# Kernel optimization log

Hardware: AMD Instinct MI355X
Metric: run time of the kernel (lower is better)

The kernel has to match this reference:

```python
import jax, jax.numpy as jnp
import numpy as np

N_WORDS = 8192   # total words across all concepts
L = 24           # chars per word (padded)
D = 256          # word_vec_d
H = 8            # attention heads
DFF = 1024
VOCAB = 128
N_CONCEPTS = 1024
MAXW = 16        # max_words
GROUPS = 4       # n_names: 4 equal groups of concepts


def setup_inputs() -> dict:
    key = jax.random.key(0)
    ks = jax.random.split(key, 9)
    rng = np.random.default_rng(0)
    # char tokens in [1, VOCAB), ragged word lengths in [4, L], tail = 0 (pad)
    vals = rng.integers(1, VOCAB, size=(N_WORDS, L))
    lens = rng.integers(4, L + 1, size=(N_WORDS,))
    inputs = np.where(np.arange(L)[None, :] < lens[:, None], vals, 0)
    # ragged words-per-concept: alternate 4 / 12 -> sums to N_WORDS, <= MAXW
    counts = np.where(np.arange(N_CONCEPTS) % 2 == 0, 4, 12)
    concept_id = np.repeat(np.arange(N_CONCEPTS), counts)
    word_pos = np.concatenate([np.arange(c) for c in counts])

    def w(k, shape):
        return 0.02 * jax.random.normal(k, shape, jnp.float32)

    return {
        "inputs": jnp.asarray(inputs, jnp.int32),
        "concept_id": jnp.asarray(concept_id, jnp.int32),
        "word_pos": jnp.asarray(word_pos, jnp.int32),
        "n_concepts": N_CONCEPTS,
        "n_names": GROUPS,
        "we_emb": w(ks[0], (VOCAB, D)),
        "we_qkv": w(ks[1], (D, 3 * D)),
        "we_o": w(ks[2], (D, D)),
        "we_ff1": w(ks[3], (D, DFF)),
        "we_ff2": w(ks[4], (DFF, D)),
        "ne_qkv": w(ks[5], (D, 3 * D)),
        "ne_o": w(ks[6], (D, D)),
        "ne_ff1": w(ks[7], (D, DFF)),
        "ne_ff2": w(ks[8], (DFF, D)),
    }


def _ln(x):
    m = x.mean(-1, keepdims=True)
    v = ((x - m) ** 2).mean(-1, keepdims=True)
    return (x - m) * jax.lax.rsqrt(v + 1e-5)


def _mha(x, wqkv, wo, key_pad=None):
    n, l, d = x.shape
    hd = d // H
    q, k, v = jnp.split(x @ wqkv, 3, axis=-1)
    q = q.reshape(n, l, H, hd)
    k = k.reshape(n, l, H, hd)
    v = v.reshape(n, l, H, hd)
    s = jnp.einsum('nqhd,nkhd->nhqk', q, k) / jnp.sqrt(jnp.asarray(hd, x.dtype))
    if key_pad is not None:
        s = jnp.where(key_pad[:, None, None, :], -1e9, s)
    a = jax.nn.softmax(s, axis=-1)
    o = jnp.einsum('nhqk,nkhd->nqhd', a, v).reshape(n, l, d)
    return o @ wo


def _block(x, wqkv, wo, w1, w2, key_pad=None):
    h = _ln(x + _mha(x, wqkv, wo, key_pad))
    return _ln(h + jax.nn.relu(h @ w1) @ w2)


def reference(inputs, concept_id, word_pos, n_concepts, n_names,
              we_emb, we_qkv, we_o, we_ff1, we_ff2,
              ne_qkv, ne_o, ne_ff1, ne_ff2):
    pad_mask = inputs == 0  # [N_WORDS, L]
    x = we_emb[inputs]      # [N_WORDS, L, D]
    word_ft = _block(x, we_qkv, we_o, we_ff1, we_ff2, pad_mask)
    # masked mean over chars -> one vector per word
    np_mask = (~pad_mask)[..., None].astype(word_ft.dtype)  # [N_WORDS, L, 1]
    name_vec = (word_ft * np_mask).sum(1) / np_mask.sum(1)   # [N_WORDS, D]
    # ragged -> padded: one scatter instead of per-sample torch.cat
    padded = jnp.zeros((n_concepts, MAXW, name_vec.shape[-1]), name_vec.dtype)
    padded = padded.at[concept_id, word_pos].set(name_vec)   # [n_concepts, MAXW, D]
    name_ft = _block(padded, ne_qkv, ne_o, ne_ff1, ne_ff2)
    row_pad = (padded == 0).all(-1, keepdims=True)           # all-zero rows = pad words
    name_ft = jnp.where(row_pad, jnp.zeros((), name_ft.dtype), name_ft)
    counts = (name_ft != 0).sum(1).astype(name_ft.dtype)     # [n_concepts, D]
    pooled = name_ft.sum(1) / counts                         # [n_concepts, D]
    return tuple(jnp.split(pooled, n_names, axis=0))
```

## Files before the change

### kernel.cpp

```cpp
#include <hip/hip_runtime.h>
#include <hip/hip_bf16.h>

#define NWORDS 8192
#define LW 24
#define DIM 256
#define NHEAD 8
#define DFF 1024
#define NCONC 1024
#define MAXW 16
#define TN (NCONC * MAXW)

typedef float floatx4 __attribute__((ext_vector_type(4)));
typedef short shortx8 __attribute__((ext_vector_type(8)));

__device__ __forceinline__ float bf2f(ushort u) {
  union { uint u; float f; } v; v.u = ((uint)u) << 16; return v.f;
}
__device__ __forceinline__ ushort f2bf(float f) {
  union { float f; uint u; } v; v.f = f;
  return (ushort)((v.u + 0x7FFFu + ((v.u >> 16) & 1u)) >> 16);
}

__device__ __forceinline__ void load_lds16(const ushort* gsrc, ushort* lds) {
  __builtin_amdgcn_global_load_lds((const __attribute__((address_space(1))) void*)gsrc,
                                   (__attribute__((address_space(3))) void*)lds, 16, 0, 0);
}

#define WAIT_VM0() __builtin_amdgcn_s_waitcnt(0x0F70)
#define WAIT_LGKM0() __builtin_amdgcn_s_waitcnt(0xC07F)

#define STAGE_COL(lane) ((((lane) & 3) ^ (((lane) >> 3) & 3)) * 8)
#define FRAG_OFF(row, quad) (((row) * 32) + ((((quad) ^ (((row) >> 1) & 3))) * 8))

__global__ __launch_bounds__(256) void wprep(const float* __restrict__ W,
                                             ushort* __restrict__ WT, int K, int N) {
  int idx = blockIdx.x * 256 + threadIdx.x;
  if (idx < K * N) {
    int k = idx / N, n = idx % N;
    WT[n * K + k] = f2bf(W[idx]);
  }
}

__global__ __launch_bounds__(256) void embed4(const int* __restrict__ inputs,
                                              const float* __restrict__ we_emb,
                                              ushort* __restrict__ x, int ntok) {
  int idx = blockIdx.x * 256 + threadIdx.x;
  int t = idx >> 6, d = (idx & 63) * 4;
  if (t < ntok) {
    const float4 f = *(const float4*)&we_emb[inputs[t] * DIM + d];
    uint2 o;
    o.x = (uint)f2bf(f.x) | ((uint)f2bf(f.y) << 16);
    o.y = (uint)f2bf(f.z) | ((uint)f2bf(f.w) << 16);
    *(uint2*)&x[(size_t)t * DIM + d] = o;
  }
}

template <bool RELU>
__global__ __launch_bounds__(256) void gemm128(const ushort* __restrict__ A,
                                               const ushort* __restrict__ BT,
                                               ushort* __restrict__ C,
                                               int lda, int ldb, int ldc, int K) {
  __shared__ ushort As[2][128 * 32];
  __shared__ ushort Bs[2][128 * 32];
  const int tid = threadIdx.x;
  const int w = tid >> 6, lane = tid & 63;
  const int quad = lane >> 4, l16 = lane & 15;
  const long m0 = (long)blockIdx.y * 128;
  const long n0 = (long)blockIdx.x * 128;
  const int srow = lane >> 2;
  const int scol = STAGE_COL(lane);
  const int wr = (w >> 1) * 64, wc = (w & 1) * 64;

  floatx4 acc[4][4] = {};
  for (int k0 = 0; k0 < K; k0 += 64) {
#pragma unroll
    for (int s = 0; s < 2; s++)
#pragma unroll
      for (int i = 0; i < 2; i++) {
        int r = w * 32 + i * 16;
        load_lds16(&A[(m0 + r + srow) * lda + k0 + s * 32 + scol], &As[s][r * 32]);
        load_lds16(&BT[(n0 + r + srow) * ldb + k0 + s * 32 + scol], &Bs[s][r * 32]);
      }
    __syncthreads();
#pragma unroll
    for (int s = 0; s < 2; s++) {
      shortx8 a[4], b[4];
#pragma unroll
      for (int i = 0; i < 4; i++) a[i] = *(const shortx8*)&As[s][FRAG_OFF(wr + i * 16 + l16, quad)];
#pragma unroll
      for (int j = 0; j < 4; j++) b[j] = *(const shortx8*)&Bs[s][FRAG_OFF(wc + j * 16 + l16, quad)];
#pragma unroll
      for (int i = 0; i < 4; i++)
#pragma unroll
        for (int j = 0; j < 4; j++)
          acc[i][j] = __builtin_amdgcn_mfma_f32_16x16x32_bf16(a[i], b[j], acc[i][j], 0, 0, 0);
    }
    __syncthreads();
  }
#pragma unroll
  for (int i = 0; i < 4; i++)
#pragma unroll
    for (int j = 0; j < 4; j++)
#pragma unroll
      for (int r = 0; r < 4; r++) {
        float v = acc[i][j][r];
        if (RELU) v = fmaxf(v, 0.f);
        long m = m0 + wr + i * 16 + quad * 4 + r;
        long n = n0 + wc + j * 16 + l16;
        C[m * ldc + n] = f2bf(v);
      }
}

__global__ __launch_bounds__(256) void gemm_ln64(const ushort* __restrict__ A, int lda,
                                                 const ushort* __restrict__ BT,
                                                 const ushort* __restrict__ RES,
                                                 ushort* __restrict__ C,
                                                 int K) {
  __shared__ ushort As[2][64 * 32];
  __shared__ ushort Bs[2][256 * 32];
  __shared__ float red1[64 * 4];
  __shared__ float red2[64 * 4];
  const int tid = threadIdx.x;
  const int w = tid >> 6, lane = tid & 63;
  const int quad = lane >> 4, l16 = lane & 15;
  const long m0 = (long)blockIdx.x * 64;
  const int srow = lane >> 2;
  const int scol = STAGE_COL(lane);
  const int wc = w * 64;

  floatx4 acc[4][4] = {};
  for (int k0 = 0; k0 < K; k0 += 64) {
#pragma unroll
    for (int s = 0; s < 2; s++) {
      load_lds16(&A[(m0 + w * 16 + srow) * lda + k0 + s * 32 + scol], &As[s][(w * 16) * 32]);
#pragma unroll
      for (int i = 0; i < 4; i++) {
        int r = w * 64 + i * 16;
        load_lds16(&BT[(long)(r + srow) * K + k0 + s * 32 + scol], &Bs[s][r * 32]);
      }
    }
    __syncthreads();
#pragma unroll
    for (int s = 0; s < 2; s++) {
      shortx8 a[4], b[4];
#pragma unroll
      for (int i = 0; i < 4; i++) a[i] = *(const shortx8*)&As[s][FRAG_OFF(i * 16 + l16, quad)];
#pragma unroll
      for (int j = 0; j < 4; j++) b[j] = *(const shortx8*)&Bs[s][FRAG_OFF(wc + j * 16 + l16, quad)];
#pragma unroll
      for (int i = 0; i < 4; i++)
#pragma unroll
        for (int j = 0; j < 4; j++)
          acc[i][j] = __builtin_amdgcn_mfma_f32_16x16x32_bf16(a[i], b[j], acc[i][j], 0, 0, 0);
    }
    __syncthreads();
  }
#pragma unroll
  for (int i = 0; i < 4; i++)
#pragma unroll
    for (int r = 0; r < 4; r++) {
      int row = i * 16 + quad * 4 + r;
      float s1 = 0.f, s2 = 0.f;
#pragma unroll
      for (int j = 0; j < 4; j++) {
        float v = acc[i][j][r] + bf2f(RES[(m0 + row) * 256 + wc + j * 16 + l16]);
        acc[i][j][r] = v;
        s1 += v;
        s2 += v * v;
      }
#pragma unroll
      for (int off = 1; off < 16; off <<= 1) {
        s1 += __shfl_xor(s1, off);
        s2 += __shfl_xor(s2, off);
      }
      if (l16 == 0) { red1[row * 4 + w] = s1; red2[row * 4 + w] = s2; }
    }
  __syncthreads();
#pragma unroll
  for (int i = 0; i < 4; i++)
#pragma unroll
    for (int r = 0; r < 4; r++) {
      int row = i * 16 + quad * 4 + r;
      float s1 = red1[row * 4] + red1[row * 4 + 1] + red1[row * 4 + 2] + red1[row * 4 + 3];
      float s2 = red2[row * 4] + red2[row * 4 + 1] + red2[row * 4 + 2] + red2[row * 4 + 3];
      float mean = s1 * (1.f / 256.f);
      float rstd = rsqrtf(s2 * (1.f / 256.f) - mean * mean + 1e-5f);
#pragma unroll
      for (int j = 0; j < 4; j++)
        C[(m0 + row) * 256 + wc + j * 16 + l16] = f2bf((acc[i][j][r] - mean) * rstd);
    }
}

__global__ __launch_bounds__(256, 2) void ffn_fused(const ushort* __restrict__ H,
                                                    const ushort* __restrict__ W1T,
                                                    const ushort* __restrict__ W2T,
                                                    ushort* __restrict__ C,
                                                    int M) {
  __shared__ __align__(16) ushort As[8 * 64 * 32];
  __shared__ __align__(16) ushort Ss[8 * 64 * 32];
  __shared__ __align__(16) ushort Wb[256 * 32];
  const int tid = threadIdx.x;
  const int w = tid >> 6, lane = tid & 63;
  const int quad = lane >> 4, l16 = lane & 15;
  const long m0 = (long)blockIdx.x * 64;
  const int srow = lane >> 2;
  const int scol = STAGE_COL(lane);

#pragma unroll
  for (int t = 0; t < 8; t++) {
    int p = 2 * w + t / 4, ii = t % 4;
    load_lds16(&H[(m0 + ii * 16 + srow) * 256 + p * 32 + scol], &As[(p * 2048) + (ii * 16) * 32]);
  }
#pragma unroll
  for (int ii = 0; ii < 4; ii++)
    load_lds16(&W1T[(long)(w * 64 + ii * 16 + srow) * 256 + scol], &Wb[(w * 64 + ii * 16) * 32]);
  __syncthreads();

  floatx4 acc2[4][4] = {};
  for (int m = 0; m < 4; m++) {
    floatx4 acc1[4][4] = {};
    if (m > 0) {
#pragma unroll
      for (int ii = 0; ii < 4; ii++)
        load_lds16(&W1T[(long)(m * 256 + w * 64 + ii * 16 + srow) * 256 + scol],
                   &Wb[(w * 64 + ii * 16) * 32]);
    }
#pragma unroll 1
    for (int p = 0; p < 8; p++) {
      WAIT_VM0();
      shortx8 a[4], b[4];
#pragma unroll
      for (int i = 0; i < 4; i++)
        a[i] = *(const shortx8*)&Wb[FRAG_OFF(w * 64 + i * 16 + l16, quad)];
      WAIT_LGKM0();
      if (p < 7) {
#pragma unroll
        for (int ii = 0; ii < 4; ii++)
          load_lds16(&W1T[(long)(m * 256 + w * 64 + ii * 16 + srow) * 256 + (p + 1) * 32 + scol],
                     &Wb[(w * 64 + ii * 16) * 32]);
      }
#pragma unroll
      for (int j = 0; j < 4; j++)
        b[j] = *(const shortx8*)&As[p * 2048 + FRAG_OFF(j * 16 + l16, quad)];
#pragma unroll
      for (int i = 0; i < 4; i++)
#pragma unroll
        for (int j = 0; j < 4; j++)
          acc1[i][j] = __builtin_amdgcn_mfma_f32_16x16x32_bf16(a[i], b[j], acc1[i][j], 0, 0, 0);
    }
    __syncthreads();
#pragma unroll
    for (int i = 0; i < 4; i++) {
      int fb = w * 64 + i * 16 + quad * 4;
      int pf = fb >> 5, c = (fb >> 3) & 3, off = fb & 7;
#pragma unroll
      for (int j = 0; j < 4; j++) {
        int tok = j * 16 + l16;
        ushort4 pk;
        pk.x = f2bf(fmaxf(acc1[i][j][0], 0.f));
        pk.y = f2bf(fmaxf(acc1[i][j][1], 0.f));
        pk.z = f2bf(fmaxf(acc1[i][j][2], 0.f));
        pk.w = f2bf(fmaxf(acc1[i][j][3], 0.f));
        *(ushort4*)&Ss[(pf * 64 + tok) * 32 + ((c ^ ((tok >> 1) & 3)) << 3) + off] = pk;
      }
    }
    __syncthreads();
#pragma unroll
    for (int jj = 0; jj < 4; jj++)
      load_lds16(&W2T[(long)(w * 64 + jj * 16 + srow) * 1024 + m * 256 + scol],
                 &Wb[(w * 64 + jj * 16) * 32]);
#pragma unroll 1
    for (int p = 0; p < 8; p++) {
      WAIT_VM0();
      shortx8 a[4], b[4];
#pragma unroll
      for (int j = 0; j < 4; j++)
        b[j] = *(const shortx8*)&Wb[FRAG_OFF(w * 64 + j * 16 + l16, quad)];
      WAIT_LGKM0();
      if (p < 7) {
#pragma unroll
        for (int jj = 0; jj < 4; jj++)
          load_lds16(&W2T[(long)(w * 64 + jj * 16 + srow) * 1024 + m * 256 + (p + 1) * 32 + scol],
                     &Wb[(w * 64 + jj * 16) * 32]);
      }
#pragma unroll
      for (int i = 0; i < 4; i++)
        a[i] = *(const shortx8*)&Ss[p * 2048 + FRAG_OFF(i * 16 + l16, quad)];
#pragma unroll
      for (int i = 0; i < 4; i++)
#pragma unroll
        for (int j = 0; j < 4; j++)
          acc2[i][j] = __builtin_amdgcn_mfma_f32_16x16x32_bf16(a[i], b[j], acc2[i][j], 0, 0, 0);
    }
  }
  __syncthreads();

  float* red1 = (float*)Ss;
  float* red2 = red1 + 256;
  const int wc = w * 64;
#pragma unroll
  for (int i = 0; i < 4; i++)
#pragma unroll
    for (int r = 0; r < 4; r++) {
      int row = i * 16 + quad * 4 + r;
      float s1 = 0.f, s2 = 0.f;
#pragma unroll
      for (int j = 0; j < 4; j++) {
        float v = acc2[i][j][r] + bf2f(H[(m0 + row) * 256 + wc + j * 16 + l16]);
        acc2[i][j][r] = v;
        s1 += v;
        s2 += v * v;
      }
#pragma unroll
      for (int off = 1; off < 16; off <<= 1) {
        s1 += __shfl_xor(s1, off);
        s2 += __shfl_xor(s2, off);
      }
      if (l16 == 0) { red1[row * 4 + w] = s1; red2[row * 4 + w] = s2; }
    }
  __syncthreads();
#pragma unroll
  for (int i = 0; i < 4; i++)
#pragma unroll
    for (int r = 0; r < 4; r++) {
      int row = i * 16 + quad * 4 + r;
      float s1 = red1[row * 4] + red1[row * 4 + 1] + red1[row * 4 + 2] + red1[row * 4 + 3];
      float s2 = red2[row * 4] + red2[row * 4 + 1] + red2[row * 4 + 2] + red2[row * 4 + 3];
      float mean = s1 * (1.f / 256.f);
      float rstd = rsqrtf(s2 * (1.f / 256.f) - mean * mean + 1e-5f);
      if (m0 + row < M) {
#pragma unroll
        for (int j = 0; j < 4; j++)
          C[(m0 + row) * 256 + wc + j * 16 + l16] = f2bf((acc2[i][j][r] - mean) * rstd);
      }
    }
}

template <int LSEQ, bool MASKED>
__global__ __launch_bounds__(256) void attn(const int* __restrict__ inputs,
                                            ushort* __restrict__ qkv) {
  __shared__ ushort Qs[LSEQ * 256];
  __shared__ ushort Ks[LSEQ * 256];
  __shared__ ushort Vs[LSEQ * 256];
  __shared__ float pads[LSEQ];
  const int blk = blockIdx.x;
  const int tid = threadIdx.x;
  ushort* base = qkv + (size_t)blk * LSEQ * 768;
  const uint4* src = (const uint4*)base;
  for (int i = tid; i < LSEQ * 96; i += 256) {
    int c = i / 96, part = i % 96;
    uint4 val = src[c * 96 + part];
    int sect = part >> 5, off = part & 31;
    ushort* dst = (sect == 0) ? Qs : (sect == 1 ? Ks : Vs);
    *(uint4*)&dst[c * 256 + off * 8] = val;
  }
  if (MASKED) {
    if (tid < LSEQ) pads[tid] = (inputs[blk * LSEQ + tid] == 0) ? 1.f : 0.f;
  }
  __syncthreads();
  if (tid < LSEQ * NHEAD) {
    const int i = tid % LSEQ, hh = tid / LSEQ;
    const int hb = hh * 32;
    float q[32];
    {
      const uint4* qr = (const uint4*)&Qs[i * 256 + hb];
#pragma unroll
      for (int u = 0; u < 4; u++) {
        uint4 ch = qr[u];
        const ushort* us = (const ushort*)&ch;
#pragma unroll
        for (int d = 0; d < 8; d++) q[u * 8 + d] = bf2f(us[d]);
      }
    }
    float s[LSEQ];
    float mx = -3e38f;
#pragma unroll
    for (int j = 0; j < LSEQ; j++) {
      const uint4* kr = (const uint4*)&Ks[j * 256 + hb];
      float a = 0.f;
#pragma unroll
      for (int u = 0; u < 4; u++) {
        uint4 ch = kr[u];
        const ushort* us = (const ushort*)&ch;
#pragma unroll
        for (int d = 0; d < 8; d++) a += q[u * 8 + d] * bf2f(us[d]);
      }
      a *= 0.17677669529663687f;
      if (MASKED && pads[j] != 0.f) a = -1e9f;
      s[j] = a;
      mx = fmaxf(mx, a);
    }
    float den = 0.f;
#pragma unroll
    for (int j = 0; j < LSEQ; j++) { s[j] = __expf(s[j] - mx); den += s[j]; }
    float inv = 1.f / den;
    float o[32] = {};
#pragma unroll
    for (int j = 0; j < LSEQ; j++) {
      float a = s[j] * inv;
      const uint4* vr = (const uint4*)&Vs[j * 256 + hb];
#pragma unroll
      for (int u = 0; u < 4; u++) {
        uint4 ch = vr[u];
        const ushort* us = (const ushort*)&ch;
#pragma unroll
        for (int d = 0; d < 8; d++) o[u * 8 + d] += a * bf2f(us[d]);
      }
    }
    ushort* orow = base + (size_t)i * 768 + hb;
#pragma unroll
    for (int d = 0; d < 32; d++) orow[d] = f2bf(o[d]);
  }
}

__global__ __launch_bounds__(256) void pool_scatter(const ushort* __restrict__ ft,
                                                    const int* __restrict__ inputs,
                                                    const int* __restrict__ cid,
                                                    const int* __restrict__ wpos,
                                                    ushort* __restrict__ padded,
                                                    int* __restrict__ flags) {
  int w = blockIdx.x, d = threadIdx.x;
  float s = 0.f;
  int cnt = 0;
  for (int c = 0; c < LW; c++) {
    if (inputs[w * LW + c] != 0) {
      s += bf2f(ft[((size_t)w * LW + c) * DIM + d]);
      cnt++;
    }
  }
  int slot = cid[w] * MAXW + wpos[w];
  padded[(size_t)slot * DIM + d] = f2bf(s / (float)cnt);
  if (d == 0) flags[slot] = 1;
}

__global__ __launch_bounds__(256) void final_pool(const ushort* __restrict__ nft,
                                                  const int* __restrict__ flags,
                                                  float* __restrict__ out) {
  int n = blockIdx.x, d = threadIdx.x;
  float s = 0.f;
  int cnt = 0;
  for (int wd = 0; wd < MAXW; wd++) {
    if (flags[n * MAXW + wd]) {
      s += bf2f(nft[((size_t)n * MAXW + wd) * DIM + d]);
      cnt++;
    }
  }
  out[n * DIM + d] = s / (float)cnt;
}

extern "C" void kernel_launch(void* const* d_in, const int* in_sizes, int n_in,
                              void* d_out, int out_size, void* d_ws, size_t ws_size,
                              hipStream_t stream) {
  const int* inputs = (const int*)d_in[0];
  const int* cid = (const int*)d_in[1];
  const int* wpos = (const int*)d_in[2];
  const float* we_emb = (const float*)d_in[5];
  const float* we_qkv = (const float*)d_in[6];
  const float* we_o = (const float*)d_in[7];
  const float* we_ff1 = (const float*)d_in[8];
  const float* we_ff2 = (const float*)d_in[9];
  const float* ne_qkv = (const float*)d_in[10];
  const float* ne_o = (const float*)d_in[11];
  const float* ne_ff1 = (const float*)d_in[12];
  const float* ne_ff2 = (const float*)d_in[13];
  float* out = (float*)d_out;

  int chunks = 4;
  if (ws_size >= 515000000UL) chunks = 1;
  else if (ws_size >= 263258112UL) chunks = 2;
  const int wpc = NWORDS / chunks;
  const int tpc = wpc * LW;

  const size_t X = (size_t)tpc * DIM * 2;
  const size_t Q = (size_t)tpc * 768 * 2;

  char* base = (char*)d_ws;
  ushort* x = (ushort*)(base);
  ushort* qkv = (ushort*)(base + X);
  ushort* h = (ushort*)(base + X + Q);
  ushort* ft = qkv;
  size_t pend = X + Q + X;
  ushort* padded = (ushort*)(base + pend);
  int* flags = (int*)(base + pend + 8388608);
  ushort* wT = (ushort*)(base + pend + 8454144);
  ushort* nqkv = (ushort*)(base);
  ushort* nh = (ushort*)(base + 25165824);
  ushort* nft = (ushort*)(base + 33554432);

  ushort* wqkvT = wT;
  ushort* woT = wT + 196608;
  ushort* wff1T = wT + 262144;
  ushort* wff2T = wT + 524288;
  ushort* nqkvT = wT + 786432;
  ushort* neoT = wT + 983040;
  ushort* neff1T = wT + 1048576;
  ushort* neff2T = wT + 1310720;

  wprep<<<768, 256, 0, stream>>>(we_qkv, wqkvT, 256, 768);
  wprep<<<256, 256, 0, stream>>>(we_o, woT, 256, 256);
  wprep<<<1024, 256, 0, stream>>>(we_ff1, wff1T, 256, 1024);
  wprep<<<1024, 256, 0, stream>>>(we_ff2, wff2T, 1024, 256);
  wprep<<<768, 256, 0, stream>>>(ne_qkv, nqkvT, 256, 768);
  wprep<<<256, 256, 0, stream>>>(ne_o, neoT, 256, 256);
  wprep<<<1024, 256, 0, stream>>>(ne_ff1, neff1T, 256, 1024);
  wprep<<<1024, 256, 0, stream>>>(ne_ff2, neff2T, 1024, 256);

  (void)hipMemsetAsync(padded, 0, (size_t)TN * DIM * 2, stream);
  (void)hipMemsetAsync(flags, 0, TN * 4, stream);

  for (int c = 0; c < chunks; c++) {
    const int* in_c = inputs + (size_t)c * wpc * LW;
    const int* cid_c = cid + (size_t)c * wpc;
    const int* wpos_c = wpos + (size_t)c * wpc;

    embed4<<<tpc / 4, 256, 0, stream>>>(in_c, we_emb, x, tpc);
    gemm128<false><<<dim3(6, tpc / 128), 256, 0, stream>>>(x, wqkvT, qkv, 256, 256, 768, 256);
    attn<24, true><<<wpc, 256, 0, stream>>>(in_c, qkv);
    gemm_ln64<<<tpc / 64, 256, 0, stream>>>(qkv, 768, woT, x, h, 256);
    ffn_fused<<<tpc / 64, 256, 0, stream>>>(h, wff1T, wff2T, ft, tpc);
    pool_scatter<<<wpc, 256, 0, stream>>>(ft, in_c, cid_c, wpos_c, padded, flags);
  }

  gemm128<false><<<dim3(6, TN / 128), 256, 0, stream>>>(padded, nqkvT, nqkv, 256, 256, 768, 256);
  attn<16, false><<<NCONC, 256, 0, stream>>>(nullptr, nqkv);
  gemm_ln64<<<TN / 64, 256, 0, stream>>>(nqkv, 768, neoT, padded, nh, 256);
  ffn_fused<<<TN / 64, 256, 0, stream>>>(nh, neff1T, neff2T, nft, TN);
  final_pool<<<NCONC, 256, 0, stream>>>(nft, flags, out);
}
```

Before: 980.2 us.

## Unify QKV and out-proj GEMMs into a 64-row kernel staging full-K activations

```diff
diff --git a/kernel.cpp b/kernel.cpp
--- a/kernel.cpp
+++ b/kernel.cpp
@@ -55,106 +55,72 @@
   }
 }
 
-template <bool RELU>
-__global__ __launch_bounds__(256) void gemm128(const ushort* __restrict__ A,
-                                               const ushort* __restrict__ BT,
-                                               ushort* __restrict__ C,
-                                               int lda, int ldb, int ldc, int K) {
-  __shared__ ushort As[2][128 * 32];
-  __shared__ ushort Bs[2][128 * 32];
-  const int tid = threadIdx.x;
-  const int w = tid >> 6, lane = tid & 63;
-  const int quad = lane >> 4, l16 = lane & 15;
-  const long m0 = (long)blockIdx.y * 128;
-  const long n0 = (long)blockIdx.x * 128;
-  const int srow = lane >> 2;
-  const int scol = STAGE_COL(lane);
-  const int wr = (w >> 1) * 64, wc = (w & 1) * 64;
-
-  floatx4 acc[4][4] = {};
-  for (int k0 = 0; k0 < K; k0 += 64) {
-#pragma unroll
-    for (int s = 0; s < 2; s++)
-#pragma unroll
-      for (int i = 0; i < 2; i++) {
-        int r = w * 32 + i * 16;
-        load_lds16(&A[(m0 + r + srow) * lda + k0 + s * 32 + scol], &As[s][r * 32]);
-        load_lds16(&BT[(n0 + r + srow) * ldb + k0 + s * 32 + scol], &Bs[s][r * 32]);
-      }
-    __syncthreads();
-#pragma unroll
-    for (int s = 0; s < 2; s++) {
-      shortx8 a[4], b[4];
-#pragma unroll
-      for (int i = 0; i < 4; i++) a[i] = *(const shortx8*)&As[s][FRAG_OFF(wr + i * 16 + l16, quad)];
-#pragma unroll
-      for (int j = 0; j < 4; j++) b[j] = *(const shortx8*)&Bs[s][FRAG_OFF(wc + j * 16 + l16, quad)];
-#pragma unroll
-      for (int i = 0; i < 4; i++)
-#pragma unroll
-        for (int j = 0; j < 4; j++)
-          acc[i][j] = __builtin_amdgcn_mfma_f32_16x16x32_bf16(a[i], b[j], acc[i][j], 0, 0, 0);
-    }
-    __syncthreads();
-  }
-#pragma unroll
-  for (int i = 0; i < 4; i++)
-#pragma unroll
-    for (int j = 0; j < 4; j++)
-#pragma unroll
-      for (int r = 0; r < 4; r++) {
-        float v = acc[i][j][r];
-        if (RELU) v = fmaxf(v, 0.f);
-        long m = m0 + wr + i * 16 + quad * 4 + r;
-        long n = n0 + wc + j * 16 + l16;
-        C[m * ldc + n] = f2bf(v);
-      }
-}
-
-__global__ __launch_bounds__(256) void gemm_ln64(const ushort* __restrict__ A, int lda,
-                                                 const ushort* __restrict__ BT,
-                                                 const ushort* __restrict__ RES,
-                                                 ushort* __restrict__ C,
-                                                 int K) {
-  __shared__ ushort As[2][64 * 32];
-  __shared__ ushort Bs[2][256 * 32];
+template <bool LN>
+__global__ __launch_bounds__(256, 2) void gemm_tok64(const ushort* __restrict__ A, int lda,
+                                                     const ushort* __restrict__ BT,
+                                                     const ushort* __restrict__ RES,
+                                                     ushort* __restrict__ C, int ldc) {
+  __shared__ __align__(16) ushort As[8 * 64 * 32];
+  __shared__ __align__(16) ushort Wb[256 * 32];
   __shared__ float red1[64 * 4];
   __shared__ float red2[64 * 4];
   const int tid = threadIdx.x;
   const int w = tid >> 6, lane = tid & 63;
   const int quad = lane >> 4, l16 = lane & 15;
-  const long m0 = (long)blockIdx.x * 64;
+  const long m0 = (long)blockIdx.y * 64;
+  const long nb = (long)blockIdx.x * 256;
   const int srow = lane >> 2;
   const int scol = STAGE_COL(lane);
   const int wc = w * 64;
 
+#pragma unroll
+  for (int t = 0; t < 8; t++) {
+    int p = 2 * w + t / 4, ii = t % 4;
+    load_lds16(&A[(m0 + ii * 16 + srow) * lda + p * 32 + scol], &As[p * 2048 + (ii * 16) * 32]);
+  }
+#pragma unroll
+  for (int ii = 0; ii < 4; ii++)
+    load_lds16(&BT[(nb + wc + ii * 16 + srow) * 256 + scol], &Wb[(wc + ii * 16) * 32]);
+  __syncthreads();
+
   floatx4 acc[4][4] = {};
-  for (int k0 = 0; k0 < K; k0 += 64) {
-#pragma unroll
-    for (int s = 0; s < 2; s++) {
-      load_lds16(&A[(m0 + w * 16 + srow) * lda + k0 + s * 32 + scol], &As[s][(w * 16) * 32]);
-#pragma unroll
-      for (int i = 0; i < 4; i++) {
-        int r = w * 64 + i * 16;
-        load_lds16(&BT[(long)(r + srow) * K + k0 + s * 32 + scol], &Bs[s][r * 32]);
-      }
-    }
-    __syncthreads();
-#pragma unroll
-    for (int s = 0; s < 2; s++) {
-      shortx8 a[4], b[4];
-#pragma unroll
-      for (int i = 0; i < 4; i++) a[i] = *(const shortx8*)&As[s][FRAG_OFF(i * 16 + l16, quad)];
-#pragma unroll
-      for (int j = 0; j < 4; j++) b[j] = *(const shortx8*)&Bs[s][FRAG_OFF(wc + j * 16 + l16, quad)];
-#pragma unroll
-      for (int i = 0; i < 4; i++)
-#pragma unroll
-        for (int j = 0; j < 4; j++)
-          acc[i][j] = __builtin_amdgcn_mfma_f32_16x16x32_bf16(a[i], b[j], acc[i][j], 0, 0, 0);
-    }
-    __syncthreads();
-  }
+#pragma unroll 1
+  for (int p = 0; p < 8; p++) {
+    WAIT_VM0();
+    shortx8 a[4], b[4];
+#pragma unroll
+    for (int j = 0; j < 4; j++)
+      b[j] = *(const shortx8*)&Wb[FRAG_OFF(wc + j * 16 + l16, quad)];
+    WAIT_LGKM0();
+    if (p < 7) {
+#pragma unroll
+      for (int ii = 0; ii < 4; ii++)
+        load_lds16(&BT[(nb + wc + ii * 16 + srow) * 256 + (p + 1) * 32 + scol],
+                   &Wb[(wc + ii * 16) * 32]);
+    }
+#pragma unroll
+    for (int i = 0; i < 4; i++)
+      a[i] = *(const shortx8*)&As[p * 2048 + FRAG_OFF(i * 16 + l16, quad)];
+#pragma unroll
+    for (int i = 0; i < 4; i++)
+#pragma unroll
+      for (int j = 0; j < 4; j++)
+        acc[i][j] = __builtin_amdgcn_mfma_f32_16x16x32_bf16(a[i], b[j], acc[i][j], 0, 0, 0);
+  }
+
+  if (!LN) {
+#pragma unroll
+    for (int i = 0; i < 4; i++)
+#pragma unroll
+      for (int j = 0; j < 4; j++)
+#pragma unroll
+        for (int r = 0; r < 4; r++) {
+          long m = m0 + i * 16 + quad * 4 + r;
+          C[m * ldc + nb + wc + j * 16 + l16] = f2bf(acc[i][j][r]);
+        }
+    return;
+  }
+
 #pragma unroll
   for (int i = 0; i < 4; i++)
 #pragma unroll
@@ -514,16 +480,28 @@
     const int* wpos_c = wpos + (size_t)c * wpc;
 
     embed4<<<tpc / 4, 256, 0, stream>>>(in_c, we_emb, x, tpc);
-    gemm128<false><<<dim3(6, tpc / 128), 256, 0, stream>>>(x, wqkvT, qkv, 256, 256, 768, 256);
+    {
+      dim3 g(3, tpc / 64);
+      gemm_tok64<false><<<g, 256, 0, stream>>>(x, 256, wqkvT, nullptr, qkv, 768);
+    }
     attn<24, true><<<wpc, 256, 0, stream>>>(in_c, qkv);
-    gemm_ln64<<<tpc / 64, 256, 0, stream>>>(qkv, 768, woT, x, h, 256);
+    {
+      dim3 g(1, tpc / 64);
+      gemm_tok64<true><<<g, 256, 0, stream>>>(qkv, 768, woT, x, h, 256);
+    }
     ffn_fused<<<tpc / 64, 256, 0, stream>>>(h, wff1T, wff2T, ft, tpc);
     pool_scatter<<<wpc, 256, 0, stream>>>(ft, in_c, cid_c, wpos_c, padded, flags);
   }
 
-  gemm128<false><<<dim3(6, TN / 128), 256, 0, stream>>>(padded, nqkvT, nqkv, 256, 256, 768, 256);
+  {
+    dim3 g(3, TN / 64);
+    gemm_tok64<false><<<g, 256, 0, stream>>>(padded, 256, nqkvT, nullptr, nqkv, 768);
+  }
   attn<16, false><<<NCONC, 256, 0, stream>>>(nullptr, nqkv);
-  gemm_ln64<<<TN / 64, 256, 0, stream>>>(nqkv, 768, neoT, padded, nh, 256);
+  {
+    dim3 g(1, TN / 64);
+    gemm_tok64<true><<<g, 256, 0, stream>>>(nqkv, 768, neoT, padded, nh, 256);
+  }
   ffn_fused<<<TN / 64, 256, 0, stream>>>(nh, neff1T, neff2T, nft, TN);
   final_pool<<<NCONC, 256, 0, stream>>>(nft, flags, out);
 }
```

Result: no change. 966.6 us, median of 3 (-1.4%).
